# Kernel tuning notes

Hardware: AMD Instinct MI355X
Metric: run time of the kernel (lower is better)

The kernel has to match this reference:

```python
import jax, jax.numpy as jnp
import numpy as np

NUM_EXPERTS = 16
TOPK = 2
NUM_SHARED = 2


def setup_inputs() -> dict:
    key = jax.random.key(0)
    k1, k2, k3, k4 = jax.random.split(key, 4)
    B, S, D = 4, 2048, 1024
    feat = jax.random.normal(k1, (B, S, D), dtype=jnp.float32)
    router_w = jax.random.normal(k2, (NUM_EXPERTS, D), dtype=jnp.float32) * 0.02
    shared_w = jax.random.normal(k3, (NUM_SHARED * D, D), dtype=jnp.float32) * 0.02
    expert_w = jax.random.normal(k4, (NUM_EXPERTS, D, D), dtype=jnp.float32) * 0.02
    return {"feat": feat, "router_w": router_w, "shared_w": shared_w, "expert_w": expert_w}


def reference(feat, router_w, shared_w, expert_w):
    B, S, D = feat.shape
    T = B * S
    x = feat.reshape(T, D)

    # router logits [T, E]
    logits = x @ router_w.T

    # shared experts: Linear(D, ns*D) then sum over the ns chunks
    shared = (x @ shared_w.T).reshape(T, NUM_SHARED, D).sum(axis=1)

    # gate_topk with norm_probs=True: top-k logits then softmax over them
    topk_vals, topk_idx = jax.lax.top_k(logits, TOPK)       # [T, k]
    weights = jax.nn.softmax(topk_vals, axis=-1)            # [T, k]

    # balance loss (training, token-level): fi = counts/(B*S), pi = mean softmax
    scores = jax.nn.softmax(logits, axis=-1)                # [T, E]
    counts = jnp.zeros((NUM_EXPERTS,), jnp.float32).at[topk_idx.reshape(-1)].add(1.0)
    fi = counts / T
    pi = scores.mean(axis=0)
    aux_loss = jnp.sum(pi * fi)

    # dense combine-weight matrix gate[t,e] = sum_k weights[t,k] * 1[idx[t,k]==e]
    gate = jnp.zeros((T, NUM_EXPERTS), jnp.float32).at[
        jnp.arange(T)[:, None], topk_idx
    ].add(weights)

    # all-expert compute then weighted combine (dense-MoE reference)
    # expert_out[t,e,h] = sum_d x[t,d] * expert_w[e,h,d]
    expert_out = jnp.einsum('td,ehd->teh', x, expert_w)
    moe = jnp.einsum('te,teh->th', gate, expert_out)

    out = (shared + moe).reshape(B, S, D)
    return out, aux_loss
```

## Files before the change

### kernel.cpp

```cpp
#include <hip/hip_runtime.h>
#include <stdint.h>

#define T_TOK 8192
#define DDIM  1024
#define NEXP  16
#define MAXTI 208

typedef unsigned short u16;
typedef __attribute__((ext_vector_type(8))) short v8s;
typedef __attribute__((ext_vector_type(4))) float v4f;

__device__ __forceinline__ u16 f2bf(float f) {
  union { float f; unsigned u; } v; v.f = f;
  unsigned r = v.u + 0x7fffu + ((v.u >> 16) & 1u);
  return (u16)(r >> 16);
}

__device__ __forceinline__ void gload_lds16(const u16* gsrc, u16* ldst) {
  typedef __attribute__((address_space(1))) const void GV;
  typedef __attribute__((address_space(3))) void LV;
  __builtin_amdgcn_global_load_lds((GV*)(uintptr_t)gsrc, (LV*)(uintptr_t)ldst, 16, 0, 0);
}

__global__ __launch_bounds__(256) void k_cvtX(const float* __restrict__ feat,
                                              u16* __restrict__ xbT) {
  int id = blockIdx.x * 256 + threadIdx.x;
  int tok = id & 8191, kcg = id >> 13;
  const float4* s = (const float4*)(feat + (size_t)tok * DDIM + kcg * 8);
  float4 a = s[0], b = s[1];
  ushort4 o0 = {f2bf(a.x), f2bf(a.y), f2bf(a.z), f2bf(a.w)};
  ushort4 o1 = {f2bf(b.x), f2bf(b.y), f2bf(b.z), f2bf(b.w)};
  ushort4* d = (ushort4*)(xbT + (size_t)id * 8);
  d[0] = o0; d[1] = o1;
}

__global__ __launch_bounds__(256) void k_cvtW(const float* __restrict__ ew,
                                              u16* __restrict__ wt) {
  int id = blockIdx.x * 256 + threadIdx.x;
  int row = id & 127, kc = (id >> 7) & 3, kk = (id >> 9) & 31;
  int tileN = (id >> 14) & 7, e = id >> 17;
  const float4* s = (const float4*)(ew + (size_t)e * 1048576 +
                                    (size_t)(tileN * 128 + row) * DDIM + kk * 32 + kc * 8);
  float4 a = s[0], b = s[1];
  ushort4 o0 = {f2bf(a.x), f2bf(a.y), f2bf(a.z), f2bf(a.w)};
  ushort4 o1 = {f2bf(b.x), f2bf(b.y), f2bf(b.z), f2bf(b.w)};
  ushort4* d = (ushort4*)(wt + (size_t)id * 8);
  d[0] = o0; d[1] = o1;
}

__global__ __launch_bounds__(256) void k_cvtS(const float* __restrict__ sw,
                                              u16* __restrict__ wt) {
  int id = blockIdx.x * 256 + threadIdx.x;
  int row = id & 127, kc = (id >> 7) & 3, kk = (id >> 9) & 31, tileN = (id >> 14) & 7;
  int h = tileN * 128 + row;
  const float4* s0 = (const float4*)(sw + (size_t)h * DDIM + kk * 32 + kc * 8);
  const float4* s1 = (const float4*)(sw + (size_t)(1024 + h) * DDIM + kk * 32 + kc * 8);
  float4 a = s0[0], b = s0[1], c = s1[0], d4 = s1[1];
  ushort4 o0 = {f2bf(a.x + c.x), f2bf(a.y + c.y), f2bf(a.z + c.z), f2bf(a.w + c.w)};
  ushort4 o1 = {f2bf(b.x + d4.x), f2bf(b.y + d4.y), f2bf(b.z + d4.z), f2bf(b.w + d4.w)};
  ushort4* d = (ushort4*)(wt + (size_t)(16 * 131072 + id) * 8);
  d[0] = o0; d[1] = o1;
}

__global__ __launch_bounds__(256) void k_router(const float* __restrict__ x,
                                                const float* __restrict__ rw,
                                                int* __restrict__ topkI,
                                                float* __restrict__ topkW,
                                                int* __restrict__ counts,
                                                float* __restrict__ piSum) {
  __shared__ float lds_pi[NEXP];
  __shared__ int   lds_cnt[NEXP];
  int tid = threadIdx.x;
  if (tid < NEXP) { lds_pi[tid] = 0.f; lds_cnt[tid] = 0; }
  __syncthreads();
  int lane = tid & 63, wave = tid >> 6;

  for (int ti = 0; ti < 8; ++ti) {
    int t = blockIdx.x * 32 + wave * 8 + ti;
    const float* xr = x + (size_t)t * DDIM;
    float xv[16];
#pragma unroll
    for (int i = 0; i < 16; ++i) xv[i] = xr[i * 64 + lane];
    float lg[NEXP];
#pragma unroll
    for (int e = 0; e < NEXP; ++e) {
      const float* wr = rw + (size_t)e * DDIM;
      float p = 0.f;
#pragma unroll
      for (int i = 0; i < 16; ++i) p += xv[i] * wr[i * 64 + lane];
#pragma unroll
      for (int off = 32; off > 0; off >>= 1) p += __shfl_xor(p, off);
      lg[e] = p;
    }
    float mx = lg[0];
#pragma unroll
    for (int e = 1; e < NEXP; ++e) mx = fmaxf(mx, lg[e]);
    float sum = 0.f;
#pragma unroll
    for (int e = 0; e < NEXP; ++e) sum += __expf(lg[e] - mx);
    float v0 = lg[0]; int i0 = 0;
#pragma unroll
    for (int e = 1; e < NEXP; ++e) if (lg[e] > v0) { v0 = lg[e]; i0 = e; }
    float v1 = -3.0e38f; int i1 = 0;
#pragma unroll
    for (int e = 0; e < NEXP; ++e) if (e != i0 && lg[e] > v1) { v1 = lg[e]; i1 = e; }
    float e1 = __expf(v1 - v0);
    float w0 = 1.f / (1.f + e1);
    float w1 = e1 / (1.f + e1);
    if (lane == 0) {
      topkI[2 * t] = i0; topkI[2 * t + 1] = i1;
      topkW[2 * t] = w0; topkW[2 * t + 1] = w1;
      atomicAdd(&lds_cnt[i0], 1); atomicAdd(&lds_cnt[i1], 1);
    }
#pragma unroll
    for (int e = 0; e < NEXP; ++e)
      if (lane == e) atomicAdd(&lds_pi[e], __expf(lg[e] - mx) / sum);
  }
  __syncthreads();
  if (tid < NEXP) {
    atomicAdd(&counts[tid], lds_cnt[tid]);
    atomicAdd(&piSum[tid], lds_pi[tid]);
  }
}

__global__ void k_finalize(const int* __restrict__ counts, const float* __restrict__ piSum,
                           int* __restrict__ offs, int* __restrict__ tileStart,
                           int* __restrict__ cursor, float* __restrict__ outAux) {
  int lane = threadIdx.x;
  int c = (lane < NEXP) ? counts[lane] : 0;
  float p = (lane < NEXP) ? piSum[lane] : 0.f;
  int tc = (c + 127) >> 7;
  int ic = c, itc = tc;
  for (int d = 1; d < NEXP; d <<= 1) {
    int v1 = __shfl_up(ic, d), v2 = __shfl_up(itc, d);
    if (lane >= d) { ic += v1; itc += v2; }
  }
  if (lane < NEXP) {
    offs[lane] = ic - c;
    tileStart[lane] = 64 + itc - tc;
    cursor[lane] = 0;
    if (lane == NEXP - 1) { offs[NEXP] = ic; tileStart[NEXP] = 64 + itc; }
  }
  float term = (lane < NEXP) ? (p / (float)T_TOK) * ((float)c / (float)T_TOK) : 0.f;
  for (int off = 8; off; off >>= 1) term += __shfl_xor(term, off);
  if (lane == 0) outAux[0] = term;
}

__global__ __launch_bounds__(256) void k_scatter(const int* __restrict__ topkI,
                                                 const float* __restrict__ topkW,
                                                 const int* __restrict__ offs,
                                                 int* __restrict__ cursor,
                                                 int* __restrict__ rowTok,
                                                 float* __restrict__ rowW) {
  __shared__ int lcnt[NEXP], lbase[NEXP];
  int tid = threadIdx.x;
  if (tid < NEXP) lcnt[tid] = 0;
  __syncthreads();
  int p = blockIdx.x * 256 + tid;
  int e = topkI[p];
  int myLocal = atomicAdd(&lcnt[e], 1);
  __syncthreads();
  if (tid < NEXP) lbase[tid] = atomicAdd(&cursor[tid], lcnt[tid]);
  __syncthreads();
  int dst = offs[e] + lbase[e] + myLocal;
  rowTok[dst] = p >> 1;
  rowW[dst] = topkW[p];
}

__global__ __launch_bounds__(256, 4) void k_gemm(const u16* __restrict__ xbT,
                                                 const u16* __restrict__ wt,
                                                 const int* __restrict__ tileStart,
                                                 const int* __restrict__ offs,
                                                 const int* __restrict__ rowTok,
                                                 const float* __restrict__ rowW,
                                                 float* __restrict__ out) {
  __shared__ u16 As[2][4096];
  __shared__ u16 Bs[2][4096];
  int tid = threadIdx.x;
  int tileN = blockIdx.x;
  int ti = blockIdx.y;
  if (ti >= tileStart[NEXP]) return;

  int e, rowStart, offBase = 0, cnt;
  if (ti < 64) { e = NEXP; rowStart = ti * 128; cnt = T_TOK; }
  else {
    e = 0;
    while (ti >= tileStart[e + 1]) ++e;
    rowStart = (ti - tileStart[e]) * 128;
    offBase = offs[e]; cnt = offs[e + 1] - offBase;
  }

  int lane = tid & 63, wave = tid >> 6;
  int srow = tid & 127;
  int kcLo = tid >> 7;
  int tok;
  if (e == NEXP) tok = rowStart + srow;
  else tok = rowTok[offBase + min(rowStart + srow, cnt - 1)];
  const u16* aBase = xbT + (size_t)tok * 8;
  const u16* wTile = wt + (size_t)(e * 8 + tileN) * 32 * 4096;

  v4f acc[4][4];
#pragma unroll
  for (int m = 0; m < 4; ++m)
#pragma unroll
    for (int n = 0; n < 4; ++n) acc[m][n] = (v4f)0.f;

  int wm = (wave >> 1) * 64, wn = (wave & 1) * 64;
  int rsel = lane & 15;
  int q = lane >> 4;

#define STAGE(buf, kk)                                                          \
  do {                                                                          \
    gload_lds16(aBase + (size_t)((kk) * 4 + kcLo) * 65536,                      \
                &As[buf][wave * 512]);                                          \
    gload_lds16(aBase + (size_t)((kk) * 4 + kcLo + 2) * 65536,                  \
                &As[buf][2048 + wave * 512]);                                   \
    gload_lds16(wTile + (size_t)(kk) * 4096 + tid * 8, &Bs[buf][wave * 512]);   \
    gload_lds16(wTile + (size_t)(kk) * 4096 + (tid + 256) * 8,                  \
                &Bs[buf][2048 + wave * 512]);                                   \
  } while (0)

  STAGE(0, 0);
  __syncthreads();

  int cur = 0;
  for (int t = 0; t < 32; ++t) {
    if (t + 1 < 32) STAGE(cur ^ 1, t + 1);

    v8s af[4], bfr[4];
#pragma unroll
    for (int m = 0; m < 4; ++m)
      af[m] = *(const v8s*)&As[cur][(q * 128 + wm + m * 16 + rsel) * 8];
#pragma unroll
    for (int n = 0; n < 4; ++n)
      bfr[n] = *(const v8s*)&Bs[cur][(q * 128 + wn + n * 16 + rsel) * 8];
#pragma unroll
    for (int m = 0; m < 4; ++m)
#pragma unroll
      for (int n = 0; n < 4; ++n)
        acc[m][n] = __builtin_amdgcn_mfma_f32_16x16x32_bf16(af[m], bfr[n], acc[m][n], 0, 0, 0);

    __syncthreads();
    cur ^= 1;
  }
#undef STAGE

  int colBase = tileN * 128 + wn + rsel;
#pragma unroll
  for (int m = 0; m < 4; ++m) {
    int rloc = rowStart + wm + m * 16 + q * 4;
#pragma unroll
    for (int j = 0; j < 4; ++j) {
      int r = rloc + j;
      if (r < cnt) {
        int t; float w;
        if (e == NEXP) { t = r; w = 1.f; }
        else { t = rowTok[offBase + r]; w = rowW[offBase + r]; }
        float* orow = out + (size_t)t * DDIM;
#pragma unroll
        for (int n = 0; n < 4; ++n)
          atomicAdd(orow + colBase + n * 16, w * acc[m][n][j]);
      }
    }
  }
}

extern "C" void kernel_launch(void* const* d_in, const int* in_sizes, int n_in,
                              void* d_out, int out_size, void* d_ws, size_t ws_size,
                              hipStream_t stream) {
  const float* feat = (const float*)d_in[0];
  const float* rw   = (const float*)d_in[1];
  const float* sw   = (const float*)d_in[2];
  const float* ew   = (const float*)d_in[3];
  float* out = (float*)d_out;
  char* ws = (char*)d_ws;

  u16* xbT = (u16*)(ws + 0);
  u16* wt  = (u16*)(ws + 16777216);
  char* smallBase = ws + 52428800;
  int*   counts    = (int*)(smallBase + 0);
  float* piSum     = (float*)(smallBase + 64);
  int*   cursor    = (int*)(smallBase + 128);
  int*   offs      = (int*)(smallBase + 192);
  int*   tileStart = (int*)(smallBase + 320);
  int*   topkI  = (int*)(ws + 52429824);
  float* topkW  = (float*)(ws + 52495360);
  int*   rowTok = (int*)(ws + 52560896);
  float* rowW   = (float*)(ws + 52626432);

  hipMemsetAsync(smallBase, 0, 192, stream);
  hipMemsetAsync(out, 0, (size_t)out_size * sizeof(float), stream);

  k_cvtX<<<4096, 256, 0, stream>>>(feat, xbT);
  k_cvtW<<<8192, 256, 0, stream>>>(ew, wt);
  k_cvtS<<<512, 256, 0, stream>>>(sw, wt);

  k_router<<<256, 256, 0, stream>>>(feat, rw, topkI, topkW, counts, piSum);
  k_finalize<<<1, 64, 0, stream>>>(counts, piSum, offs, tileStart, cursor, out + 8388608);
  k_scatter<<<64, 256, 0, stream>>>(topkI, topkW, offs, cursor, rowTok, rowW);

  dim3 gGemm(8, MAXTI);
  k_gemm<<<gGemm, 256, 0, stream>>>(xbT, wt, tileStart, offs, rowTok, rowW, out);
}
```

Baseline: 414.0 us.

## Transpose conversions through LDS for coalescing and deepen GEMM prefetch with explicit waits

The fp32-to-bf16 conversion kernels now stage each tile through LDS, so global reads cover contiguous row segments and global writes are full 16-byte coalesced stores. The expert and shared-weight conversions are merged into one launch. The GEMM main loop issues loads for two stages ahead and replaces __syncthreads with explicit vmcnt/lgkmcnt waits, barriers and raised wave priority around the MFMA block, so memory latency overlaps with compute. The hand-tuned waitcnt values and buffer reuse must match the number of issued loads exactly, or the loop reads stale LDS data.

```diff
diff --git a/kernel.cpp b/kernel.cpp
--- a/kernel.cpp
+++ b/kernel.cpp
@@ -22,44 +22,61 @@
   __builtin_amdgcn_global_load_lds((GV*)(uintptr_t)gsrc, (LV*)(uintptr_t)ldst, 16, 0, 0);
 }
 
-__global__ __launch_bounds__(256) void k_cvtX(const float* __restrict__ feat,
+
+__global__ __launch_bounds__(256) void k_cvtA(const float* __restrict__ feat,
                                               u16* __restrict__ xbT) {
-  int id = blockIdx.x * 256 + threadIdx.x;
-  int tok = id & 8191, kcg = id >> 13;
-  const float4* s = (const float4*)(feat + (size_t)tok * DDIM + kcg * 8);
-  float4 a = s[0], b = s[1];
-  ushort4 o0 = {f2bf(a.x), f2bf(a.y), f2bf(a.z), f2bf(a.w)};
-  ushort4 o1 = {f2bf(b.x), f2bf(b.y), f2bf(b.z), f2bf(b.w)};
-  ushort4* d = (ushort4*)(xbT + (size_t)id * 8);
-  d[0] = o0; d[1] = o1;
-}
-
-__global__ __launch_bounds__(256) void k_cvtW(const float* __restrict__ ew,
+  __shared__ u16 lds[4096];
+  int b = blockIdx.x;
+  int tb = b & 63, kk = b >> 6;
+  int tid = threadIdx.x;
+  int frow = tid >> 3, fcol = tid & 7;
+#pragma unroll
+  for (int p = 0; p < 4; ++p) {
+    int row = frow + p * 32;
+    float4 v = *(const float4*)(feat + (size_t)(tb * 128 + row) * DDIM + kk * 32 + fcol * 4);
+    ushort4 o = {f2bf(v.x), f2bf(v.y), f2bf(v.z), f2bf(v.w)};
+    *(ushort4*)&lds[((fcol >> 1) * 128 + row) * 8 + (fcol & 1) * 4] = o;
+  }
+  __syncthreads();
+#pragma unroll
+  for (int i = 0; i < 2; ++i) {
+    int s = tid + i * 256;
+    u16* dst = xbT + ((size_t)(kk * 4 + (s >> 7)) * 8192 + tb * 128 + (s & 127)) * 8;
+    *(float4*)dst = *(float4*)&lds[s * 8];
+  }
+}
+
+__global__ __launch_bounds__(256) void k_cvtB(const float* __restrict__ ew,
+                                              const float* __restrict__ sw,
                                               u16* __restrict__ wt) {
-  int id = blockIdx.x * 256 + threadIdx.x;
-  int row = id & 127, kc = (id >> 7) & 3, kk = (id >> 9) & 31;
-  int tileN = (id >> 14) & 7, e = id >> 17;
-  const float4* s = (const float4*)(ew + (size_t)e * 1048576 +
-                                    (size_t)(tileN * 128 + row) * DDIM + kk * 32 + kc * 8);
-  float4 a = s[0], b = s[1];
-  ushort4 o0 = {f2bf(a.x), f2bf(a.y), f2bf(a.z), f2bf(a.w)};
-  ushort4 o1 = {f2bf(b.x), f2bf(b.y), f2bf(b.z), f2bf(b.w)};
-  ushort4* d = (ushort4*)(wt + (size_t)id * 8);
-  d[0] = o0; d[1] = o1;
-}
-
-__global__ __launch_bounds__(256) void k_cvtS(const float* __restrict__ sw,
-                                              u16* __restrict__ wt) {
-  int id = blockIdx.x * 256 + threadIdx.x;
-  int row = id & 127, kc = (id >> 7) & 3, kk = (id >> 9) & 31, tileN = (id >> 14) & 7;
-  int h = tileN * 128 + row;
-  const float4* s0 = (const float4*)(sw + (size_t)h * DDIM + kk * 32 + kc * 8);
-  const float4* s1 = (const float4*)(sw + (size_t)(1024 + h) * DDIM + kk * 32 + kc * 8);
-  float4 a = s0[0], b = s0[1], c = s1[0], d4 = s1[1];
-  ushort4 o0 = {f2bf(a.x + c.x), f2bf(a.y + c.y), f2bf(a.z + c.z), f2bf(a.w + c.w)};
-  ushort4 o1 = {f2bf(b.x + d4.x), f2bf(b.y + d4.y), f2bf(b.z + d4.z), f2bf(b.w + d4.w)};
-  ushort4* d = (ushort4*)(wt + (size_t)(16 * 131072 + id) * 8);
-  d[0] = o0; d[1] = o1;
+  __shared__ u16 lds[4096];
+  int b = blockIdx.x;
+  int kk = b & 31, tileN = (b >> 5) & 7, e = b >> 8;
+  int tid = threadIdx.x;
+  int frow = tid >> 3, fcol = tid & 7;
+#pragma unroll
+  for (int p = 0; p < 4; ++p) {
+    int row = frow + p * 32;
+    float4 v;
+    if (e < NEXP) {
+      v = *(const float4*)(ew + ((size_t)e << 20) + (size_t)(tileN * 128 + row) * DDIM +
+                           kk * 32 + fcol * 4);
+    } else {
+      int h = tileN * 128 + row;
+      float4 a = *(const float4*)(sw + (size_t)h * DDIM + kk * 32 + fcol * 4);
+      float4 c = *(const float4*)(sw + (size_t)(1024 + h) * DDIM + kk * 32 + fcol * 4);
+      v = make_float4(a.x + c.x, a.y + c.y, a.z + c.z, a.w + c.w);
+    }
+    ushort4 o = {f2bf(v.x), f2bf(v.y), f2bf(v.z), f2bf(v.w)};
+    *(ushort4*)&lds[((fcol >> 1) * 128 + row) * 8 + (fcol & 1) * 4] = o;
+  }
+  __syncthreads();
+  u16* dst = wt + (size_t)((e * 8 + tileN) * 32 + kk) * 4096;
+#pragma unroll
+  for (int i = 0; i < 2; ++i) {
+    int s = tid + i * 256;
+    *(float4*)&dst[s * 8] = *(float4*)&lds[s * 8];
+  }
 }
 
 __global__ __launch_bounds__(256) void k_router(const float* __restrict__ x,
@@ -220,30 +237,58 @@
                 &Bs[buf][2048 + wave * 512]);                                   \
   } while (0)
 
+#define LOADFRAGS(buf)                                                          \
+  do {                                                                          \
+    _Pragma("unroll")                                                           \
+    for (int m = 0; m < 4; ++m)                                                 \
+      af[m] = *(const v8s*)&As[buf][(q * 128 + wm + m * 16 + rsel) * 8];        \
+    _Pragma("unroll")                                                           \
+    for (int n = 0; n < 4; ++n)                                                 \
+      bfr[n] = *(const v8s*)&Bs[buf][(q * 128 + wn + n * 16 + rsel) * 8];       \
+  } while (0)
+
+#define DOMFMA                                                                  \
+  do {                                                                          \
+    _Pragma("unroll")                                                           \
+    for (int m = 0; m < 4; ++m)                                                 \
+      _Pragma("unroll")                                                         \
+      for (int n = 0; n < 4; ++n)                                               \
+        acc[m][n] = __builtin_amdgcn_mfma_f32_16x16x32_bf16(af[m], bfr[n],      \
+                                                            acc[m][n], 0, 0, 0);\
+  } while (0)
+
+  v8s af[4], bfr[4];
+
   STAGE(0, 0);
-  __syncthreads();
+  STAGE(1, 1);
 
   int cur = 0;
-  for (int t = 0; t < 32; ++t) {
-    if (t + 1 < 32) STAGE(cur ^ 1, t + 1);
-
-    v8s af[4], bfr[4];
-#pragma unroll
-    for (int m = 0; m < 4; ++m)
-      af[m] = *(const v8s*)&As[cur][(q * 128 + wm + m * 16 + rsel) * 8];
-#pragma unroll
-    for (int n = 0; n < 4; ++n)
-      bfr[n] = *(const v8s*)&Bs[cur][(q * 128 + wn + n * 16 + rsel) * 8];
-#pragma unroll
-    for (int m = 0; m < 4; ++m)
-#pragma unroll
-      for (int n = 0; n < 4; ++n)
-        acc[m][n] = __builtin_amdgcn_mfma_f32_16x16x32_bf16(af[m], bfr[n], acc[m][n], 0, 0, 0);
-
-    __syncthreads();
+  for (int t = 0; t < 31; ++t) {
+    asm volatile("s_waitcnt vmcnt(4)" ::: "memory");
+    __builtin_amdgcn_s_barrier();
+    __builtin_amdgcn_sched_barrier(0);
+    LOADFRAGS(cur);
+    asm volatile("s_waitcnt lgkmcnt(0)" ::: "memory");
+    __builtin_amdgcn_sched_barrier(0);
+    __builtin_amdgcn_s_barrier();
+    __builtin_amdgcn_sched_barrier(0);
+    if (t < 30) STAGE(cur, t + 2);
+    __builtin_amdgcn_s_setprio(1);
+    DOMFMA;
+    __builtin_amdgcn_s_setprio(0);
     cur ^= 1;
   }
+  asm volatile("s_waitcnt vmcnt(0)" ::: "memory");
+  __builtin_amdgcn_s_barrier();
+  __builtin_amdgcn_sched_barrier(0);
+  LOADFRAGS(cur);
+  asm volatile("s_waitcnt lgkmcnt(0)" ::: "memory");
+  __builtin_amdgcn_sched_barrier(0);
+  DOMFMA;
+
 #undef STAGE
+#undef LOADFRAGS
+#undef DOMFMA
 
   int colBase = tileN * 128 + wn + rsel;
 #pragma unroll
@@ -291,9 +336,8 @@
   hipMemsetAsync(smallBase, 0, 192, stream);
   hipMemsetAsync(out, 0, (size_t)out_size * sizeof(float), stream);
 
-  k_cvtX<<<4096, 256, 0, stream>>>(feat, xbT);
-  k_cvtW<<<8192, 256, 0, stream>>>(ew, wt);
-  k_cvtS<<<512, 256, 0, stream>>>(sw, wt);
+  k_cvtA<<<2048, 256, 0, stream>>>(feat, xbT);
+  k_cvtB<<<4352, 256, 0, stream>>>(ew, sw, wt);
 
   k_router<<<256, 256, 0, stream>>>(feat, rw, topkI, topkW, counts, piSum);
   k_finalize<<<1, 64, 0, stream>>>(counts, piSum, offs, tileStart, cursor, out + 8388608);
```

Result: no change. 407.0 us (-1.7%).
